# Optimization experiments

Hardware: AMD Instinct MI355X
Metric: run time of the kernel (lower is better)

## Reference

```python
import jax, jax.numpy as jnp
import numpy as np

WS = 8
NH = 6

def _ln(x, g, b, eps=1e-5):
    m = x.mean(-1, keepdims=True)
    v = jnp.var(x, axis=-1, keepdims=True)
    return (x - m) / jnp.sqrt(v + eps) * g + b

def _dwconv(x_nchw, k):
    # depthwise 3x3, stride 1, padding 1 (SAME); k: (C,1,3,3)
    return jax.lax.conv_general_dilated(
        x_nchw, k, (1, 1), 'SAME',
        dimension_numbers=('NCHW', 'OIHW', 'NCHW'),
        feature_group_count=x_nchw.shape[1])

def setup_inputs() -> dict:
    key = jax.random.key(0)
    ks = jax.random.split(key, 12)
    B, H, W, C = 2, 256, 256, 180
    hd_ffn = 360
    s = 0.02
    return {
        'x': jax.random.normal(ks[0], (B, H * W, C), jnp.float32),
        'w_qkv': jax.random.normal(ks[1], (3 * C, C), jnp.float32) * s,
        'b_rel': jax.random.normal(ks[2], (NH, WS * WS, WS * WS), jnp.float32) * s,
        'w_proj': jax.random.normal(ks[3], (C, C), jnp.float32) * s,
        'b_proj': jnp.zeros((C,), jnp.float32),
        'conv_dw': jax.random.normal(ks[4], (C, 1, 3, 3), jnp.float32) * 0.1,
        'cg_w1': jax.random.normal(ks[5], (C // 8, C), jnp.float32) * s,
        'cg_w2': jax.random.normal(ks[6], (C, C // 8), jnp.float32) * s,
        'ffn_w1': jax.random.normal(ks[7], (hd_ffn, C), jnp.float32) * s,
        'ffn_dw': jax.random.normal(ks[8], (hd_ffn, 1, 3, 3), jnp.float32) * 0.1,
        'ffn_w2': jax.random.normal(ks[9], (C, hd_ffn), jnp.float32) * s,
        'n1_g': jnp.ones((C,), jnp.float32),
        'n1_b': jnp.zeros((C,), jnp.float32),
        'n2_g': jnp.ones((C,), jnp.float32),
        'n2_b': jnp.zeros((C,), jnp.float32),
        'H': H,
        'W': W,
    }

def reference(x, w_qkv, b_rel, w_proj, b_proj, conv_dw, cg_w1, cg_w2,
              ffn_w1, ffn_dw, ffn_w2, n1_g, n1_b, n2_g, n2_b, H, W):
    B, L, C = x.shape
    hd = C // NH
    scale = hd ** -0.5
    n1 = _ln(x, n1_g, n1_b)
    # --- spatial window attention branch ---
    xw = n1.reshape(B, H // WS, WS, W // WS, WS, C)
    xw = xw.transpose(0, 1, 3, 2, 4, 5).reshape(-1, WS * WS, C)  # (nw, 64, C)
    qkv = (xw @ w_qkv.T).reshape(-1, WS * WS, 3, NH, hd).transpose(2, 0, 3, 1, 4)
    q, k, v = qkv[0], qkv[1], qkv[2]  # (nw, nh, 64, hd)
    attn = jax.nn.softmax((q * scale) @ jnp.swapaxes(k, -2, -1) + b_rel, axis=-1)
    out = (attn @ v).transpose(0, 2, 1, 3).reshape(-1, WS * WS, C)
    out = out @ w_proj.T + b_proj
    attn_feat = out.reshape(B, H // WS, W // WS, WS, WS, C)
    attn_feat = attn_feat.transpose(0, 1, 3, 2, 4, 5).reshape(B, L, C)
    # --- conv branch: depthwise 3x3 + GELU ---
    nchw = n1.transpose(0, 2, 1).reshape(B, C, H, W)
    conv_feat = jax.nn.gelu(_dwconv(nchw, conv_dw), approximate=False)
    conv_feat = conv_feat.reshape(B, C, L).transpose(0, 2, 1)
    # --- AIM: channel gate on conv_feat modulates attn_feat ---
    pooled = conv_feat.mean(axis=1)  # (B, C) == AdaptiveAvgPool2d(1)
    cm = jax.nn.sigmoid(jax.nn.gelu(pooled @ cg_w1.T, approximate=False) @ cg_w2.T)
    x = x + (attn_feat * cm[:, None, :] + conv_feat)
    # --- FFN with depthwise spatial mixing ---
    n2 = _ln(x, n2_g, n2_b)
    h = jax.nn.gelu(n2 @ ffn_w1.T, approximate=False)  # (B, L, hd_ffn)
    hdim = h.shape[-1]
    h_s = _dwconv(h.transpose(0, 2, 1).reshape(B, hdim, H, W), ffn_dw)
    h_s = h_s.reshape(B, hdim, L).transpose(0, 2, 1)
    return x + h_s @ ffn_w2.T
```

## Files before the change

### kernel.cpp

```cpp
#include <hip/hip_runtime.h>
#include <hip/hip_bf16.h>
#include <math.h>

#define BATCH 2
#define IMG 256
#define LTOK 65536
#define CH 180
#define BL (BATCH * LTOK)
#define HDF 360

using frag_ab = __attribute__((ext_vector_type(8))) short;
using frag_cd = __attribute__((ext_vector_type(4))) float;

__device__ __forceinline__ float b2f(unsigned short u) {
    union { unsigned int i; float f; } v; v.i = ((unsigned int)u) << 16; return v.f;
}
__device__ __forceinline__ float blo(unsigned int u) {
    union { unsigned int i; float f; } v; v.i = u << 16; return v.f;
}
__device__ __forceinline__ float bhi(unsigned int u) {
    union { unsigned int i; float f; } v; v.i = u & 0xffff0000u; return v.f;
}
__device__ __forceinline__ unsigned short f2b(float f) {
    union { float f; unsigned int i; } v; v.f = f;
    unsigned int x = v.i;
    unsigned int r = (x + 0x7fffu + ((x >> 16) & 1u)) >> 16;
    return (unsigned short)r;
}
__device__ __forceinline__ float gelu_f(float x) {
    return 0.5f * x * (1.0f + erff(x * 0.70710678118654752f));
}

template <int PERM>
__device__ __forceinline__ int perm_row(int row) {
    if (PERM == 1) {
        int b = row >> 16, l = row & 65535;
        int y = l >> 8, x = l & 255;
        return (b << 16) + ((((y >> 3) << 5) + (x >> 3)) << 6) + ((y & 7) << 3) + (x & 7);
    } else if (PERM == 2) {
        int b = row >> 16, wv = row & 65535;
        int wid = wv >> 6, t = wv & 63;
        int wy = wid >> 5, wx = wid & 31;
        return (b << 16) + ((((wy << 3) + (t >> 3))) << 8) + (wx << 3) + (t & 7);
    }
    return row;
}

__global__ __launch_bounds__(256) void convw_kernel(
    const float* __restrict__ a, const float* __restrict__ b,
    const float* __restrict__ c, const float* __restrict__ d,
    const float* __restrict__ cdw, const float* __restrict__ fdw,
    const float* __restrict__ brel,
    unsigned short* __restrict__ wbf, float* __restrict__ wT1, float* __restrict__ wT2,
    unsigned short* __restrict__ br3)
{
    int g = blockIdx.x * 256 + threadIdx.x;
    if (g < 259200) {
        float v;
        if      (g < 97200)  v = a[g];
        else if (g < 129600) v = b[g - 97200];
        else if (g < 194400) v = c[g - 129600];
        else                 v = d[g - 194400];
        wbf[g] = f2b(v);
    } else if (g < 265680) {
        int i = g - 259200;
        int tap = i / 180, ch = i % 180;
        wT1[i] = cdw[ch * 9 + tap];
    } else if (g < 278640) {
        int i = g - 265680;
        int tap = i / 360, ch = i % 360;
        wT2[i] = fdw[ch * 9 + tap];
    } else if (g < 303216) {
        int i = g - 278640;
        int h = i >> 12;
        int rem = i & 4095;
        int lane = rem >> 6;
        int j = rem & 63;
        int mt = j >> 4, nt = (j >> 2) & 3, r = j & 3;
        int row = mt * 16 + (lane >> 4) * 4 + r;
        int col = nt * 16 + (lane & 15);
        br3[i] = f2b(brel[h * 4096 + row * 64 + col]);
    }
}

__device__ __forceinline__ void ld4(const float* p, float v[4]) {
    float4 t = *(const float4*)p; v[0]=t.x; v[1]=t.y; v[2]=t.z; v[3]=t.w;
}
__device__ __forceinline__ void ld4(const unsigned short* p, float v[4]) {
    ushort4 t = *(const ushort4*)p; v[0]=b2f(t.x); v[1]=b2f(t.y); v[2]=b2f(t.z); v[3]=b2f(t.w);
}

template <typename TIN>
__global__ __launch_bounds__(256) void ln_kernel(
    const TIN* __restrict__ x, const float* __restrict__ g,
    const float* __restrict__ bta, unsigned short* __restrict__ out)
{
    int wave = threadIdx.x >> 6, lane = threadIdx.x & 63;
    int tok = blockIdx.x * 4 + wave;
    const bool act = lane < 45;
    float v[4] = {0.f, 0.f, 0.f, 0.f};
    const TIN* row = x + (size_t)tok * CH;
    if (act) ld4(row + lane * 4, v);
    float s  = v[0] + v[1] + v[2] + v[3];
    float sq = v[0]*v[0] + v[1]*v[1] + v[2]*v[2] + v[3]*v[3];
    #pragma unroll
    for (int off = 32; off > 0; off >>= 1) {
        s  += __shfl_xor(s, off);
        sq += __shfl_xor(sq, off);
    }
    float mean = s * (1.f / CH);
    float var  = sq * (1.f / CH) - mean * mean;
    float rstd = rsqrtf(var + 1e-5f);
    if (act) {
        float4 gg = *(const float4*)&g[lane * 4];
        float4 bb = *(const float4*)&bta[lane * 4];
        unsigned int o0 = (unsigned int)f2b((v[0]-mean)*rstd*gg.x + bb.x)
                        | ((unsigned int)f2b((v[1]-mean)*rstd*gg.y + bb.y) << 16);
        unsigned int o1 = (unsigned int)f2b((v[2]-mean)*rstd*gg.z + bb.z)
                        | ((unsigned int)f2b((v[3]-mean)*rstd*gg.w + bb.w) << 16);
        *(uint2*)(out + (size_t)tok * CH + lane * 4) = make_uint2(o0, o1);
    }
}

__device__ __forceinline__ void stv(float* p, float v) { *p = v; }
__device__ __forceinline__ void stv(unsigned short* p, float v) { *p = f2b(v); }

template <int ACT, bool HAS_BIAS, bool HAS_RES, int PERM, typename TOUT>
__global__ __launch_bounds__(256) void gemm_kernel(
    const unsigned short* __restrict__ X, int ldx,
    const unsigned short* __restrict__ Wt,
    const float* __restrict__ bias,
    const unsigned short* __restrict__ res, int ldr,
    TOUT* __restrict__ Y, int ldy,
    int N, int K)
{
    __shared__ unsigned short Xs[256][40];
    __shared__ unsigned short Ws[64][40];
    const int tid = threadIdx.x;
    const int wave = tid >> 6;
    const int lane = tid & 63;
    const int l16 = lane & 15;
    const int q = lane >> 4;
    const int n0 = blockIdx.x * 64;
    const int m0 = blockIdx.y * 256;
    const int lr = tid >> 2;
    const int lk = (tid & 3) << 3;

    frag_cd acc[4][4];
    #pragma unroll
    for (int mb = 0; mb < 4; ++mb)
        #pragma unroll
        for (int nb = 0; nb < 4; ++nb)
            acc[mb][nb] = (frag_cd){0.f, 0.f, 0.f, 0.f};

    for (int k0 = 0; k0 < K; k0 += 32) {
        const bool kfull = (k0 + 32 <= K);
        #pragma unroll
        for (int rr = 0; rr < 4; ++rr) {
            const int row = rr * 64 + lr;
            const unsigned short* p = X + (size_t)(m0 + row) * ldx + (k0 + lk);
            if (kfull) {
                uint2 u0 = *(const uint2*)p;
                uint2 u1 = *(const uint2*)(p + 4);
                *(uint4*)&Xs[row][lk] = make_uint4(u0.x, u0.y, u1.x, u1.y);
            } else {
                #pragma unroll
                for (int j = 0; j < 8; ++j)
                    Xs[row][lk + j] = (k0 + lk + j < K) ? p[j] : (unsigned short)0;
            }
        }
        {
            const int n = n0 + lr;
            const unsigned short* p = Wt + (size_t)n * K + (k0 + lk);
            if (n < N && kfull) {
                uint2 u0 = *(const uint2*)p;
                uint2 u1 = *(const uint2*)(p + 4);
                *(uint4*)&Ws[lr][lk] = make_uint4(u0.x, u0.y, u1.x, u1.y);
            } else {
                #pragma unroll
                for (int j = 0; j < 8; ++j)
                    Ws[lr][lk + j] = (n < N && (k0 + lk + j) < K) ? p[j] : (unsigned short)0;
            }
        }
        __syncthreads();
        frag_ab bfr[4];
        #pragma unroll
        for (int nb = 0; nb < 4; ++nb)
            bfr[nb] = *(const frag_ab*)&Ws[nb * 16 + l16][q * 8];
        #pragma unroll
        for (int mb = 0; mb < 4; ++mb) {
            frag_ab afr = *(const frag_ab*)&Xs[wave * 64 + mb * 16 + l16][q * 8];
            #pragma unroll
            for (int nb = 0; nb < 4; ++nb)
                acc[mb][nb] = __builtin_amdgcn_mfma_f32_16x16x32_bf16(afr, bfr[nb], acc[mb][nb], 0, 0, 0);
        }
        __syncthreads();
    }
    #pragma unroll
    for (int nb = 0; nb < 4; ++nb) {
        const int col = n0 + nb * 16 + l16;
        if (col < N) {
            float bv = 0.f;
            if (HAS_BIAS) bv = bias[col];
            #pragma unroll
            for (int mb = 0; mb < 4; ++mb) {
                #pragma unroll
                for (int r = 0; r < 4; ++r) {
                    int row = m0 + wave * 64 + mb * 16 + q * 4 + r;
                    int orow = perm_row<PERM>(row);
                    float v = acc[mb][nb][r] + bv;
                    if (ACT == 1) v = gelu_f(v);
                    if (HAS_RES) v += b2f(res[(size_t)orow * ldr + col]);
                    stv(&Y[(size_t)orow * ldy + col], v);
                }
            }
        }
    }
}

__global__ __launch_bounds__(64) void attn_kernel(
    const unsigned short* __restrict__ qkvw,
    const unsigned short* __restrict__ br3,
    unsigned short* __restrict__ attn_out)
{
    __shared__ unsigned short Pl[64][72];
    __shared__ unsigned short VT[32][72];
    const int blk = blockIdx.x;
    const int h = blk % 6;
    const int w = blk / 6;
    const int lane = threadIdx.x;
    const int l16 = lane & 15;
    const int g4 = lane >> 4;
    const float scale = 0.18257418583505536f;

    const unsigned short* base = qkvw + (size_t)w * (64 * 540) + h * 30;

    frag_ab qf[4], kf[4];
    #pragma unroll
    for (int t = 0; t < 4; ++t) {
        const unsigned short* pq = base + (size_t)(t * 16 + l16) * 540 + g4 * 8;
        union { frag_ab f; uint2 u[2]; } tq, tk;
        tq.u[0] = *(const uint2*)pq;        tq.u[1] = *(const uint2*)(pq + 4);
        tk.u[0] = *(const uint2*)(pq + 180); tk.u[1] = *(const uint2*)(pq + 184);
        if (g4 == 3) { tk.f[6] = 0; tk.f[7] = 0; }
        qf[t] = tq.f; kf[t] = tk.f;
    }

    unsigned int brw[32];
    {
        const unsigned short* bp = br3 + ((size_t)h << 12) + lane * 64;
        #pragma unroll
        for (int c2 = 0; c2 < 8; ++c2)
            *(uint4*)&brw[c2 * 4] = *(const uint4*)(bp + c2 * 8);
    }

    frag_cd s[4][4];
    #pragma unroll
    for (int mt = 0; mt < 4; ++mt)
        #pragma unroll
        for (int nt = 0; nt < 4; ++nt)
            s[mt][nt] = (frag_cd){0.f, 0.f, 0.f, 0.f};
    #pragma unroll
    for (int mt = 0; mt < 4; ++mt)
        #pragma unroll
        for (int nt = 0; nt < 4; ++nt)
            s[mt][nt] = __builtin_amdgcn_mfma_f32_16x16x32_bf16(qf[mt], kf[nt], s[mt][nt], 0, 0, 0);

    {
        const unsigned short* pv = base + (size_t)lane * 540 + 360;
        #pragma unroll
        for (int d2 = 0; d2 < 15; ++d2) {
            unsigned int u = *(const unsigned int*)(pv + 2 * d2);
            VT[2 * d2][lane]     = (unsigned short)(u & 0xffffu);
            VT[2 * d2 + 1][lane] = (unsigned short)(u >> 16);
        }
        VT[30][lane] = 0; VT[31][lane] = 0;
    }

    float inv[4][4];
    #pragma unroll
    for (int mt = 0; mt < 4; ++mt) {
        #pragma unroll
        for (int r = 0; r < 4; ++r) {
            float a0 = s[mt][0][r] * scale + (((0 * 4 + r) & 1) ? bhi(brw[(mt * 16 + 0 + r) >> 1]) : blo(brw[(mt * 16 + 0 + r) >> 1]));
            float a1 = s[mt][1][r] * scale + (((1 * 4 + r) & 1) ? bhi(brw[(mt * 16 + 4 + r) >> 1]) : blo(brw[(mt * 16 + 4 + r) >> 1]));
            float a2 = s[mt][2][r] * scale + (((2 * 4 + r) & 1) ? bhi(brw[(mt * 16 + 8 + r) >> 1]) : blo(brw[(mt * 16 + 8 + r) >> 1]));
            float a3 = s[mt][3][r] * scale + (((3 * 4 + r) & 1) ? bhi(brw[(mt * 16 + 12 + r) >> 1]) : blo(brw[(mt * 16 + 12 + r) >> 1]));
            float m = fmaxf(fmaxf(a0, a1), fmaxf(a2, a3));
            m = fmaxf(m, __shfl_xor(m, 1));
            m = fmaxf(m, __shfl_xor(m, 2));
            m = fmaxf(m, __shfl_xor(m, 4));
            m = fmaxf(m, __shfl_xor(m, 8));
            float e0 = __expf(a0 - m), e1 = __expf(a1 - m);
            float e2 = __expf(a2 - m), e3 = __expf(a3 - m);
            float sum = e0 + e1 + e2 + e3;
            sum += __shfl_xor(sum, 1);
            sum += __shfl_xor(sum, 2);
            sum += __shfl_xor(sum, 4);
            sum += __shfl_xor(sum, 8);
            inv[mt][r] = 1.f / sum;
            int row = mt * 16 + g4 * 4 + r;
            Pl[row][l16]      = f2b(e0);
            Pl[row][16 + l16] = f2b(e1);
            Pl[row][32 + l16] = f2b(e2);
            Pl[row][48 + l16] = f2b(e3);
        }
    }
    __syncthreads();

    frag_ab pf[4][2];
    #pragma unroll
    for (int mt = 0; mt < 4; ++mt)
        #pragma unroll
        for (int kt = 0; kt < 2; ++kt)
            pf[mt][kt] = *(const frag_ab*)&Pl[mt * 16 + l16][kt * 32 + g4 * 8];
    frag_ab vf[2][2];
    #pragma unroll
    for (int nt = 0; nt < 2; ++nt)
        #pragma unroll
        for (int kt = 0; kt < 2; ++kt)
            vf[nt][kt] = *(const frag_ab*)&VT[nt * 16 + l16][kt * 32 + g4 * 8];

    frag_cd o[4][2];
    #pragma unroll
    for (int mt = 0; mt < 4; ++mt)
        #pragma unroll
        for (int nt = 0; nt < 2; ++nt)
            o[mt][nt] = (frag_cd){0.f, 0.f, 0.f, 0.f};
    #pragma unroll
    for (int mt = 0; mt < 4; ++mt)
        #pragma unroll
        for (int nt = 0; nt < 2; ++nt)
            #pragma unroll
            for (int kt = 0; kt < 2; ++kt)
                o[mt][nt] = __builtin_amdgcn_mfma_f32_16x16x32_bf16(pf[mt][kt], vf[nt][kt], o[mt][nt], 0, 0, 0);

    unsigned short* ob = attn_out + (size_t)w * (64 * CH) + h * 30;
    #pragma unroll
    for (int mt = 0; mt < 4; ++mt) {
        #pragma unroll
        for (int r = 0; r < 4; ++r) {
            int row = mt * 16 + g4 * 4 + r;
            float iv = inv[mt][r];
            unsigned short* op = ob + (size_t)row * CH;
            op[l16] = f2b(o[mt][0][r] * iv);
            if (l16 < 14) op[16 + l16] = f2b(o[mt][1][r] * iv);
        }
    }
}

template <int C, bool DO_GELU>
__global__ __launch_bounds__(256) void dwconv_kernel(
    const unsigned short* __restrict__ in, const float* __restrict__ wT,
    unsigned short* __restrict__ out)
{
    constexpr int NG = (C + 7) / 8;
    constexpr int TY = 8;
    int gid = blockIdx.x * 256 + threadIdx.x;
    int cg = gid % NG;
    int t  = gid / NG;
    int x  = t % IMG;
    int t2 = t / IMG;
    int yb = t2 & 31;
    int bi = t2 >> 5;
    if (bi >= BATCH) return;
    const int c0 = cg * 8;
    const int y0 = yb * TY;

    float w9[9][8];
    #pragma unroll
    for (int tp = 0; tp < 9; ++tp) {
        float4 wa = *(const float4*)&wT[tp * C + c0];
        float4 wb = *(const float4*)&wT[tp * C + c0 + 4];
        w9[tp][0]=wa.x; w9[tp][1]=wa.y; w9[tp][2]=wa.z; w9[tp][3]=wa.w;
        w9[tp][4]=wb.x; w9[tp][5]=wb.y; w9[tp][6]=wb.z; w9[tp][7]=wb.w;
    }

    unsigned int rr[3][3][4];

    auto load_row = [&](int y, unsigned int dst[3][4]) {
        if ((unsigned)y >= (unsigned)IMG) {
            #pragma unroll
            for (int cc = 0; cc < 3; ++cc)
                #pragma unroll
                for (int k = 0; k < 4; ++k) dst[cc][k] = 0u;
            return;
        }
        size_t base = ((size_t)((bi << 16) + (y << 8) + x)) * C + c0;
        #pragma unroll
        for (int cc = 0; cc < 3; ++cc) {
            int xx = x + cc - 1;
            if ((unsigned)xx >= (unsigned)IMG) {
                dst[cc][0] = dst[cc][1] = dst[cc][2] = dst[cc][3] = 0u;
                continue;
            }
            const unsigned short* p = in + base + (ptrdiff_t)(cc - 1) * C;
            uint2 u0 = *(const uint2*)p;
            uint2 u1 = *(const uint2*)(p + 4);
            dst[cc][0] = u0.x; dst[cc][1] = u0.y; dst[cc][2] = u1.x; dst[cc][3] = u1.y;
        }
    };

    load_row(y0 - 1, rr[0]);
    load_row(y0,     rr[1]);

    #pragma unroll
    for (int dy = 0; dy < TY; ++dy) {
        load_row(y0 + dy + 1, rr[(dy + 2) % 3]);
        float acc[8];
        #pragma unroll
        for (int j = 0; j < 8; ++j) acc[j] = 0.f;
        #pragma unroll
        for (int ky = 0; ky < 3; ++ky) {
            unsigned int (*row)[4] = rr[(dy + ky) % 3];
            #pragma unroll
            for (int kx = 0; kx < 3; ++kx) {
                const float* wp = w9[ky * 3 + kx];
                const unsigned int* u = row[kx];
                acc[0] += blo(u[0]) * wp[0];
                acc[1] += bhi(u[0]) * wp[1];
                acc[2] += blo(u[1]) * wp[2];
                acc[3] += bhi(u[1]) * wp[3];
                acc[4] += blo(u[2]) * wp[4];
                acc[5] += bhi(u[2]) * wp[5];
                acc[6] += blo(u[3]) * wp[6];
                acc[7] += bhi(u[3]) * wp[7];
            }
        }
        if (DO_GELU) {
            #pragma unroll
            for (int j = 0; j < 8; ++j) acc[j] = gelu_f(acc[j]);
        }
        size_t ob = ((size_t)((bi << 16) + ((y0 + dy) << 8) + x)) * C + c0;
        unsigned int o0 = (unsigned int)f2b(acc[0]) | ((unsigned int)f2b(acc[1]) << 16);
        unsigned int o1 = (unsigned int)f2b(acc[2]) | ((unsigned int)f2b(acc[3]) << 16);
        *(uint2*)(out + ob) = make_uint2(o0, o1);
        if (c0 + 8 <= C) {
            unsigned int o2 = (unsigned int)f2b(acc[4]) | ((unsigned int)f2b(acc[5]) << 16);
            unsigned int o3 = (unsigned int)f2b(acc[6]) | ((unsigned int)f2b(acc[7]) << 16);
            *(uint2*)(out + ob + 4) = make_uint2(o2, o3);
        }
    }
}

__global__ __launch_bounds__(64) void pool_kernel(
    const unsigned short* __restrict__ cf, float* __restrict__ pooled)
{
    int t = threadIdx.x;
    if (t >= 45) return;
    int b = blockIdx.x >> 7;
    int chunk = blockIdx.x & 127;
    const unsigned short* base = cf + (size_t)(b * LTOK + chunk * 512) * CH + t * 4;
    float s0 = 0.f, s1 = 0.f, s2 = 0.f, s3 = 0.f;
    for (int i = 0; i < 512; ++i) {
        ushort4 v = *(const ushort4*)(base + (size_t)i * CH);
        s0 += b2f(v.x); s1 += b2f(v.y); s2 += b2f(v.z); s3 += b2f(v.w);
    }
    atomicAdd(&pooled[b * CH + t * 4 + 0], s0);
    atomicAdd(&pooled[b * CH + t * 4 + 1], s1);
    atomicAdd(&pooled[b * CH + t * 4 + 2], s2);
    atomicAdd(&pooled[b * CH + t * 4 + 3], s3);
}

__global__ __launch_bounds__(256) void cm_kernel(
    const float* __restrict__ pooled, const float* __restrict__ w1,
    const float* __restrict__ w2, float* __restrict__ cm)
{
    __shared__ float p[BATCH][CH];
    __shared__ float g1[BATCH][22];
    int t = threadIdx.x;
    for (int idx = t; idx < BATCH * CH; idx += 256)
        p[idx / CH][idx % CH] = pooled[idx] * (1.f / (float)LTOK);
    __syncthreads();
    if (t < BATCH * 22) {
        int b = t / 22, u = t % 22;
        float s = 0.f;
        for (int c = 0; c < CH; ++c) s += p[b][c] * w1[u * CH + c];
        g1[b][u] = gelu_f(s);
    }
    __syncthreads();
    for (int idx = t; idx < BATCH * CH; idx += 256) {
        int b = idx / CH, c = idx % CH;
        float s = 0.f;
        for (int u = 0; u < 22; ++u) s += g1[b][u] * w2[c * 22 + u];
        cm[idx] = 1.f / (1.f + __expf(-s));
    }
}

__global__ __launch_bounds__(256) void resid_kernel(
    const float* __restrict__ x, const unsigned short* __restrict__ attn_feat,
    const unsigned short* __restrict__ conv_feat, const float* __restrict__ cm,
    unsigned short* __restrict__ x_mid)
{
    int gid = blockIdx.x * 256 + threadIdx.x;
    int c4 = gid % 45;
    int b = gid / (LTOK * 45);
    float4 xv = ((const float4*)x)[gid];
    ushort4 a = ((const ushort4*)attn_feat)[gid];
    ushort4 c = ((const ushort4*)conv_feat)[gid];
    float4 m = *(const float4*)&cm[b * CH + c4 * 4];
    unsigned int o0 = (unsigned int)f2b(xv.x + b2f(a.x) * m.x + b2f(c.x))
                    | ((unsigned int)f2b(xv.y + b2f(a.y) * m.y + b2f(c.y)) << 16);
    unsigned int o1 = (unsigned int)f2b(xv.z + b2f(a.z) * m.z + b2f(c.z))
                    | ((unsigned int)f2b(xv.w + b2f(a.w) * m.w + b2f(c.w)) << 16);
    ((uint2*)x_mid)[gid] = make_uint2(o0, o1);
}

extern "C" void kernel_launch(void* const* d_in, const int* in_sizes, int n_in,
                              void* d_out, int out_size, void* d_ws, size_t ws_size,
                              hipStream_t stream)
{
    const float* x       = (const float*)d_in[0];
    const float* w_qkv   = (const float*)d_in[1];
    const float* b_rel   = (const float*)d_in[2];
    const float* w_proj  = (const float*)d_in[3];
    const float* b_proj  = (const float*)d_in[4];
    const float* conv_dw = (const float*)d_in[5];
    const float* cg_w1   = (const float*)d_in[6];
    const float* cg_w2   = (const float*)d_in[7];
    const float* ffn_w1  = (const float*)d_in[8];
    const float* ffn_dw  = (const float*)d_in[9];
    const float* ffn_w2  = (const float*)d_in[10];
    const float* n1_g    = (const float*)d_in[11];
    const float* n1_b    = (const float*)d_in[12];
    const float* n2_g    = (const float*)d_in[13];
    const float* n2_b    = (const float*)d_in[14];

    char* ws = (char*)d_ws;
    unsigned short* n1        = (unsigned short*)(ws);
    unsigned short* qkvw      = (unsigned short*)(ws + 47185920);
    unsigned short* conv_feat = (unsigned short*)(ws + 188743680);
    unsigned short* attn_out  = (unsigned short*)(ws);
    unsigned short* attn_feat = (unsigned short*)(ws + 47185920);
    unsigned short* x_mid     = (unsigned short*)(ws + 94371840);
    unsigned short* n2        = (unsigned short*)(ws + 141557760);
    unsigned short* h         = (unsigned short*)(ws);
    unsigned short* h_s       = (unsigned short*)(ws + 141557760);
    float*          pooled    = (float*)(ws + 235929600);
    float*          cmv       = (float*)(ws + 235931040);
    unsigned short* wbf       = (unsigned short*)(ws + 235932480);
    float*          wT1       = (float*)(ws + 236450880);
    float*          wT2       = (float*)(ws + 236476800);
    unsigned short* br3       = (unsigned short*)(ws + 236528640);
    unsigned short* wqkv_b  = wbf;
    unsigned short* wproj_b = wbf + 97200;
    unsigned short* wffn1_b = wbf + 129600;
    unsigned short* wffn2_b = wbf + 194400;
    float* out = (float*)d_out;

    hipMemsetAsync(pooled, 0, 2880, stream);

    convw_kernel<<<1185, 256, 0, stream>>>(w_qkv, w_proj, ffn_w1, ffn_w2,
                                           conv_dw, ffn_dw, b_rel, wbf, wT1, wT2, br3);
    ln_kernel<float><<<BL / 4, 256, 0, stream>>>(x, n1_g, n1_b, n1);
    gemm_kernel<0, false, false, 1, unsigned short><<<dim3(9, BL / 256), 256, 0, stream>>>(
        n1, CH, wqkv_b, nullptr, nullptr, 0, qkvw, 540, 540, CH);
    dwconv_kernel<CH, true><<<1472, 256, 0, stream>>>(n1, wT1, conv_feat);
    pool_kernel<<<BATCH * 128, 64, 0, stream>>>(conv_feat, pooled);
    cm_kernel<<<1, 256, 0, stream>>>(pooled, cg_w1, cg_w2, cmv);
    attn_kernel<<<2048 * 6, 64, 0, stream>>>(qkvw, br3, attn_out);
    gemm_kernel<0, true, false, 2, unsigned short><<<dim3(3, BL / 256), 256, 0, stream>>>(
        attn_out, CH, wproj_b, b_proj, nullptr, 0, attn_feat, CH, CH, CH);
    resid_kernel<<<(BL * CH / 4) / 256, 256, 0, stream>>>(x, attn_feat, conv_feat, cmv, x_mid);
    ln_kernel<unsigned short><<<BL / 4, 256, 0, stream>>>(x_mid, n2_g, n2_b, n2);
    gemm_kernel<1, false, false, 0, unsigned short><<<dim3(6, BL / 256), 256, 0, stream>>>(
        n2, CH, wffn1_b, nullptr, nullptr, 0, h, HDF, HDF, CH);
    dwconv_kernel<HDF, false><<<2880, 256, 0, stream>>>(h, wT2, h_s);
    gemm_kernel<0, false, true, 0, float><<<dim3(3, BL / 256), 256, 0, stream>>>(
        h_s, HDF, wffn2_b, nullptr, x_mid, CH, out, CH, CH, HDF);
}
```

Before: 1.052 ms.

## Drop LDS staging in GEMM and loop each block over all N tiles

The GEMM kernel no longer stages X and W tiles through shared memory with two barriers per K step. Each wave now loads its MFMA A and B fragments straight from global memory. Each block covers 128 rows and loops internally over every 64-column N tile, so the activation rows are reused through cache and the grid becomes one-dimensional. This removes LDS traffic and block synchronisation, but adds repeated global fragment loads with poor coalescing and no software prefetch. Weight rows past N are read without a bounds guard; those reads land in the workspace and their results are masked on store.

```diff
diff --git a/kernel.cpp b/kernel.cpp
--- a/kernel.cpp
+++ b/kernel.cpp
@@ -125,6 +125,20 @@
 __device__ __forceinline__ void stv(float* p, float v) { *p = v; }
 __device__ __forceinline__ void stv(unsigned short* p, float v) { *p = f2b(v); }
 
+__device__ __forceinline__ frag_ab ldg_frag(const unsigned short* p) {
+    union { frag_ab f; uint2 u[2]; } t;
+    t.u[0] = *(const uint2*)p;
+    t.u[1] = *(const uint2*)(p + 4);
+    return t.f;
+}
+__device__ __forceinline__ frag_ab ldg_frag_tail(const unsigned short* p, int kcol0, int K) {
+    union { frag_ab f; unsigned short s[8]; } t;
+    #pragma unroll
+    for (int j = 0; j < 8; ++j)
+        t.s[j] = (kcol0 + j < K) ? p[j] : (unsigned short)0;
+    return t.f;
+}
+
 template <int ACT, bool HAS_BIAS, bool HAS_RES, int PERM, typename TOUT>
 __global__ __launch_bounds__(256) void gemm_kernel(
     const unsigned short* __restrict__ X, int ldx,
@@ -134,84 +148,70 @@
     TOUT* __restrict__ Y, int ldy,
     int N, int K)
 {
-    __shared__ unsigned short Xs[256][40];
-    __shared__ unsigned short Ws[64][40];
     const int tid = threadIdx.x;
     const int wave = tid >> 6;
     const int lane = tid & 63;
     const int l16 = lane & 15;
     const int q = lane >> 4;
-    const int n0 = blockIdx.x * 64;
-    const int m0 = blockIdx.y * 256;
-    const int lr = tid >> 2;
-    const int lk = (tid & 3) << 3;
-
-    frag_cd acc[4][4];
-    #pragma unroll
-    for (int mb = 0; mb < 4; ++mb)
+    const int m0 = blockIdx.x * 128;
+
+    const unsigned short* aptr0 = X + (size_t)(m0 + wave * 32 + l16) * ldx + q * 8;
+    const unsigned short* aptr1 = aptr0 + (size_t)16 * ldx;
+
+    const int KF = K & ~31;
+    const int ktail0 = KF + q * 8;
+
+    for (int n0 = 0; n0 < N; n0 += 64) {
+        frag_cd acc[2][4];
+        #pragma unroll
+        for (int mb = 0; mb < 2; ++mb)
+            #pragma unroll
+            for (int nb = 0; nb < 4; ++nb)
+                acc[mb][nb] = (frag_cd){0.f, 0.f, 0.f, 0.f};
+
+        const unsigned short* bptr[4];
         #pragma unroll
         for (int nb = 0; nb < 4; ++nb)
-            acc[mb][nb] = (frag_cd){0.f, 0.f, 0.f, 0.f};
-
-    for (int k0 = 0; k0 < K; k0 += 32) {
-        const bool kfull = (k0 + 32 <= K);
-        #pragma unroll
-        for (int rr = 0; rr < 4; ++rr) {
-            const int row = rr * 64 + lr;
-            const unsigned short* p = X + (size_t)(m0 + row) * ldx + (k0 + lk);
-            if (kfull) {
-                uint2 u0 = *(const uint2*)p;
-                uint2 u1 = *(const uint2*)(p + 4);
-                *(uint4*)&Xs[row][lk] = make_uint4(u0.x, u0.y, u1.x, u1.y);
-            } else {
+            bptr[nb] = Wt + (size_t)(n0 + nb * 16 + l16) * K + q * 8;
+
+        for (int k0 = 0; k0 < KF; k0 += 32) {
+            frag_ab a0 = ldg_frag(aptr0 + k0);
+            frag_ab a1 = ldg_frag(aptr1 + k0);
+            #pragma unroll
+            for (int nb = 0; nb < 4; ++nb) {
+                frag_ab b = ldg_frag(bptr[nb] + k0);
+                acc[0][nb] = __builtin_amdgcn_mfma_f32_16x16x32_bf16(a0, b, acc[0][nb], 0, 0, 0);
+                acc[1][nb] = __builtin_amdgcn_mfma_f32_16x16x32_bf16(a1, b, acc[1][nb], 0, 0, 0);
+            }
+        }
+        if (KF < K) {
+            frag_ab a0 = ldg_frag_tail(aptr0 + KF, ktail0, K);
+            frag_ab a1 = ldg_frag_tail(aptr1 + KF, ktail0, K);
+            #pragma unroll
+            for (int nb = 0; nb < 4; ++nb) {
+                frag_ab b = ldg_frag_tail(bptr[nb] + KF, ktail0, K);
+                acc[0][nb] = __builtin_amdgcn_mfma_f32_16x16x32_bf16(a0, b, acc[0][nb], 0, 0, 0);
+                acc[1][nb] = __builtin_amdgcn_mfma_f32_16x16x32_bf16(a1, b, acc[1][nb], 0, 0, 0);
+            }
+        }
+
+        #pragma unroll
+        for (int nb = 0; nb < 4; ++nb) {
+            const int col = n0 + nb * 16 + l16;
+            if (col < N) {
+                float bv = 0.f;
+                if (HAS_BIAS) bv = bias[col];
                 #pragma unroll
-                for (int j = 0; j < 8; ++j)
-                    Xs[row][lk + j] = (k0 + lk + j < K) ? p[j] : (unsigned short)0;
-            }
-        }
-        {
-            const int n = n0 + lr;
-            const unsigned short* p = Wt + (size_t)n * K + (k0 + lk);
-            if (n < N && kfull) {
-                uint2 u0 = *(const uint2*)p;
-                uint2 u1 = *(const uint2*)(p + 4);
-                *(uint4*)&Ws[lr][lk] = make_uint4(u0.x, u0.y, u1.x, u1.y);
-            } else {
-                #pragma unroll
-                for (int j = 0; j < 8; ++j)
-                    Ws[lr][lk + j] = (n < N && (k0 + lk + j) < K) ? p[j] : (unsigned short)0;
-            }
-        }
-        __syncthreads();
-        frag_ab bfr[4];
-        #pragma unroll
-        for (int nb = 0; nb < 4; ++nb)
-            bfr[nb] = *(const frag_ab*)&Ws[nb * 16 + l16][q * 8];
-        #pragma unroll
-        for (int mb = 0; mb < 4; ++mb) {
-            frag_ab afr = *(const frag_ab*)&Xs[wave * 64 + mb * 16 + l16][q * 8];
-            #pragma unroll
-            for (int nb = 0; nb < 4; ++nb)
-                acc[mb][nb] = __builtin_amdgcn_mfma_f32_16x16x32_bf16(afr, bfr[nb], acc[mb][nb], 0, 0, 0);
-        }
-        __syncthreads();
-    }
-    #pragma unroll
-    for (int nb = 0; nb < 4; ++nb) {
-        const int col = n0 + nb * 16 + l16;
-        if (col < N) {
-            float bv = 0.f;
-            if (HAS_BIAS) bv = bias[col];
-            #pragma unroll
-            for (int mb = 0; mb < 4; ++mb) {
-                #pragma unroll
-                for (int r = 0; r < 4; ++r) {
-                    int row = m0 + wave * 64 + mb * 16 + q * 4 + r;
-                    int orow = perm_row<PERM>(row);
-                    float v = acc[mb][nb][r] + bv;
-                    if (ACT == 1) v = gelu_f(v);
-                    if (HAS_RES) v += b2f(res[(size_t)orow * ldr + col]);
-                    stv(&Y[(size_t)orow * ldy + col], v);
+                for (int mb = 0; mb < 2; ++mb) {
+                    #pragma unroll
+                    for (int r = 0; r < 4; ++r) {
+                        int row = m0 + wave * 32 + mb * 16 + q * 4 + r;
+                        int orow = perm_row<PERM>(row);
+                        float v = acc[mb][nb][r] + bv;
+                        if (ACT == 1) v = gelu_f(v);
+                        if (HAS_RES) v += b2f(res[(size_t)orow * ldr + col]);
+                        stv(&Y[(size_t)orow * ldy + col], v);
+                    }
                 }
             }
         }
@@ -553,19 +553,19 @@
     convw_kernel<<<1185, 256, 0, stream>>>(w_qkv, w_proj, ffn_w1, ffn_w2,
                                            conv_dw, ffn_dw, b_rel, wbf, wT1, wT2, br3);
     ln_kernel<float><<<BL / 4, 256, 0, stream>>>(x, n1_g, n1_b, n1);
-    gemm_kernel<0, false, false, 1, unsigned short><<<dim3(9, BL / 256), 256, 0, stream>>>(
+    gemm_kernel<0, false, false, 1, unsigned short><<<BL / 128, 256, 0, stream>>>(
         n1, CH, wqkv_b, nullptr, nullptr, 0, qkvw, 540, 540, CH);
     dwconv_kernel<CH, true><<<1472, 256, 0, stream>>>(n1, wT1, conv_feat);
     pool_kernel<<<BATCH * 128, 64, 0, stream>>>(conv_feat, pooled);
     cm_kernel<<<1, 256, 0, stream>>>(pooled, cg_w1, cg_w2, cmv);
     attn_kernel<<<2048 * 6, 64, 0, stream>>>(qkvw, br3, attn_out);
-    gemm_kernel<0, true, false, 2, unsigned short><<<dim3(3, BL / 256), 256, 0, stream>>>(
+    gemm_kernel<0, true, false, 2, unsigned short><<<BL / 128, 256, 0, stream>>>(
         attn_out, CH, wproj_b, b_proj, nullptr, 0, attn_feat, CH, CH, CH);
     resid_kernel<<<(BL * CH / 4) / 256, 256, 0, stream>>>(x, attn_feat, conv_feat, cmv, x_mid);
     ln_kernel<unsigned short><<<BL / 4, 256, 0, stream>>>(x_mid, n2_g, n2_b, n2);
-    gemm_kernel<1, false, false, 0, unsigned short><<<dim3(6, BL / 256), 256, 0, stream>>>(
+    gemm_kernel<1, false, false, 0, unsigned short><<<BL / 128, 256, 0, stream>>>(
         n2, CH, wffn1_b, nullptr, nullptr, 0, h, HDF, HDF, CH);
     dwconv_kernel<HDF, false><<<2880, 256, 0, stream>>>(h, wT2, h_s);
-    gemm_kernel<0, false, true, 0, float><<<dim3(3, BL / 256), 256, 0, stream>>>(
+    gemm_kernel<0, false, true, 0, float><<<BL / 128, 256, 0, stream>>>(
         h_s, HDF, wffn2_b, nullptr, x_mid, CH, out, CH, CH, HDF);
 }
```

Result: faster. 1.002 ms (-4.7%).
